# Optimization experiments

Measured on AMD Instinct MI355X. Metric: run time of the kernel, lower is better.

## Reference

```python
import jax, jax.numpy as jnp
import numpy as np

SQRT_D = 8.0

def setup_inputs() -> dict:
    key = jax.random.key(0)
    kq, kk, kv = jax.random.split(key, 3)
    shape = (2, 16, 2048, 64)  # [batch, heads, seq, head_dim]
    return {
        "q": jax.random.normal(kq, shape, dtype=jnp.float32),
        "k": jax.random.normal(kk, shape, dtype=jnp.float32),
        "v": jax.random.normal(kv, shape, dtype=jnp.float32),
    }

def reference(q, k, v):
    # score = softmax(QK^T / sqrt_d) over the key axis j
    scores = jnp.einsum('bhif,bhjf->bhij', q, k) / SQRT_D
    probs = jax.nn.softmax(scores, axis=-1)
    # Note: original returns output permuted to [b, i, h, f]
    attn = jnp.einsum('bhij,bhjf->bihf', probs, v)
    return attn
```

## Files before the change

kernel.cpp:

```cpp
#include <hip/hip_runtime.h>

#define S_LEN 2048
#define HEADS 16
#define DIM 64

typedef __attribute__((ext_vector_type(8))) short short8;
typedef __attribute__((ext_vector_type(16))) float float16v;
typedef __attribute__((ext_vector_type(4))) float float4v;
typedef __attribute__((ext_vector_type(4))) unsigned uint4v;

static __device__ __forceinline__ unsigned pkbf(float lo, float hi) {
  unsigned r;
  asm("v_cvt_pk_bf16_f32 %0, %1, %2" : "=v"(r) : "v"(lo), "v"(hi));
  return r;
}

static __device__ __forceinline__ void gll16(const short* g, short* l) {
  __builtin_amdgcn_global_load_lds(
      (const __attribute__((address_space(1))) void*)g,
      (__attribute__((address_space(3))) void*)l, 16, 0, 0);
}

static __device__ __forceinline__ void bar() {
  asm volatile("" ::: "memory");
  __builtin_amdgcn_s_barrier();
  asm volatile("" ::: "memory");
}

__global__ __launch_bounds__(256) void prep(const float* __restrict__ kk,
                                            const float* __restrict__ vv,
                                            short* __restrict__ kb,
                                            short* __restrict__ vt) {
  __shared__ unsigned t32[64 * 33];
  const int bx = blockIdx.x;
  const int bh = bx >> 5;
  const int j0 = (bx & 31) * 64;
  const int tid = threadIdx.x;

  {
    const int j = tid >> 2, f0 = (tid & 3) * 16;
    const float4v* src = (const float4v*)(kk + ((size_t)bh * S_LEN + j0 + j) * DIM + f0);
    float4v a0 = src[0], a1 = src[1], a2 = src[2], a3 = src[3];
    uint4v w0, w1;
    w0[0] = pkbf(a0[0], a0[1]); w0[1] = pkbf(a0[2], a0[3]);
    w0[2] = pkbf(a1[0], a1[1]); w0[3] = pkbf(a1[2], a1[3]);
    w1[0] = pkbf(a2[0], a2[1]); w1[1] = pkbf(a2[2], a2[3]);
    w1[2] = pkbf(a3[0], a3[1]); w1[3] = pkbf(a3[2], a3[3]);
    short* dstb = kb + (size_t)bh * (S_LEN * DIM) +
                  ((j0 >> 5) + (j >> 5)) * 2048 + (f0 >> 4) * 512 + (j & 31) * 8;
    *(uint4v*)dstb = w0;
    *(uint4v*)(dstb + 256) = w1;
  }
  {
    const int jp = (tid & 31) * 2, f0 = (tid >> 5) * 8;
    const int pp = ((jp & ~12) | ((jp & 4) << 1) | ((jp & 8) >> 1)) >> 1;
    const float* r0 = vv + ((size_t)bh * S_LEN + j0 + jp) * DIM + f0;
    const float* r1 = r0 + DIM;
    float4v a0 = *(const float4v*)r0, a1 = *(const float4v*)(r0 + 4);
    float4v b0 = *(const float4v*)r1, b1 = *(const float4v*)(r1 + 4);
#pragma unroll
    for (int e = 0; e < 4; e++) {
      t32[(f0 + e) * 33 + pp]     = pkbf(a0[e], b0[e]);
      t32[(f0 + 4 + e) * 33 + pp] = pkbf(a1[e], b1[e]);
    }
  }
  __syncthreads();
  {
    const int f = tid >> 2, x0 = (tid & 3) * 8;
    uint4v c0 = *(const uint4v*)&t32[f * 33 + x0];
    uint4v c1 = *(const uint4v*)&t32[f * 33 + x0 + 4];
    const int jt = (j0 >> 5) + (x0 >> 4);
    const int qd = (f >> 5) * 2 + ((x0 >> 3) & 1);
    short* dstb = vt + (size_t)bh * (S_LEN * DIM) + jt * 2048 + qd * 512 + (f & 31) * 8;
    *(uint4v*)dstb = c0;
    *(uint4v*)(dstb + 256) = c1;
  }
}

__global__ __launch_bounds__(256, 2) void attn_fwd(const float* __restrict__ q,
                                                   const short* __restrict__ kb,
                                                   const short* __restrict__ vt,
                                                   float* __restrict__ out) {
  __shared__ alignas(16) short lds[16384];
  const int bx0 = blockIdx.x;
  const int bx = (bx0 & 7) * 64 + (bx0 >> 3);
  const int bh = bx >> 4, it = bx & 15;
  const int b = bh >> 4, h = bh & 15;
  const int tid = threadIdx.x;
  const int w = tid >> 6, lane = tid & 63;
  const int n = lane & 31, hf = lane >> 5;
  const int i0 = it * 128 + w * 32;

  short8 qa[4];
  {
    const float sc = 0.125f * 1.44269504088896f;
    const float* qr = q + ((size_t)bh * S_LEN + i0 + n) * DIM + hf * 8;
#pragma unroll
    for (int ks = 0; ks < 4; ks++) {
      float4v x0 = *(const float4v*)(qr + ks * 16);
      float4v x1 = *(const float4v*)(qr + ks * 16 + 4);
      uint4v pk_;
      pk_[0] = pkbf(x0[0] * sc, x0[1] * sc); pk_[1] = pkbf(x0[2] * sc, x0[3] * sc);
      pk_[2] = pkbf(x1[0] * sc, x1[1] * sc); pk_[3] = pkbf(x1[2] * sc, x1[3] * sc);
      qa[ks] = *(short8*)&pk_;
    }
  }

  const short* kbase = kb + (size_t)bh * (S_LEN * DIM);
  const short* vbase = vt + (size_t)bh * (S_LEN * DIM);

  float16v zz;
#pragma unroll
  for (int e = 0; e < 16; e++) zz[e] = 0.f;
  float16v a0 = zz, a1 = zz;
  float lpa = 0.f, lpb = 0.f;

  auto stage = [&](short* dst, int t) {
    const int jt = 2 * t;
#pragma unroll
    for (int s = 0; s < 2; ++s) {
      gll16(kbase + (size_t)(jt + s) * 2048 + w * 512 + lane * 8, dst + s * 2048 + w * 512);
      gll16(vbase + (size_t)(jt + s) * 2048 + w * 512 + lane * 8, dst + 4096 + s * 2048 + w * 512);
    }
  };

  auto compute = [&](const short* kl, const short* vl) {
    short8 kf0 = *(const short8*)(kl + lane * 8);
    short8 kf1 = *(const short8*)(kl + 512 + lane * 8);
    short8 kf2 = *(const short8*)(kl + 1024 + lane * 8);
    short8 kf3 = *(const short8*)(kl + 1536 + lane * 8);
    __builtin_amdgcn_s_setprio(1);
    float16v sa = __builtin_amdgcn_mfma_f32_32x32x16_bf16(kf0, qa[0], zz, 0, 0, 0);
    float16v sb = __builtin_amdgcn_mfma_f32_32x32x16_bf16(kf2, qa[2], zz, 0, 0, 0);
    sa = __builtin_amdgcn_mfma_f32_32x32x16_bf16(kf1, qa[1], sa, 0, 0, 0);
    sb = __builtin_amdgcn_mfma_f32_32x32x16_bf16(kf3, qa[3], sb, 0, 0, 0);
    __builtin_amdgcn_s_setprio(0);
    float16v st;
#pragma unroll
    for (int e = 0; e < 16; e++) st[e] = __builtin_amdgcn_exp2f(sa[e] + sb[e]);
#pragma unroll
    for (int e = 0; e < 8; e++) { lpa += st[2 * e]; lpb += st[2 * e + 1]; }
    uint4v pb0, pb1;
#pragma unroll
    for (int u = 0; u < 4; u++) {
      pb0[u] = pkbf(st[2 * u], st[2 * u + 1]);
      pb1[u] = pkbf(st[8 + 2 * u], st[8 + 2 * u + 1]);
    }
    short8 p0 = *(short8*)&pb0, p1 = *(short8*)&pb1;
    short8 vf0 = *(const short8*)(vl + lane * 8);
    short8 vf1 = *(const short8*)(vl + 512 + lane * 8);
    short8 vf2 = *(const short8*)(vl + 1024 + lane * 8);
    short8 vf3 = *(const short8*)(vl + 1536 + lane * 8);
    __builtin_amdgcn_s_setprio(1);
    a0 = __builtin_amdgcn_mfma_f32_32x32x16_bf16(vf0, p0, a0, 0, 0, 0);
    a1 = __builtin_amdgcn_mfma_f32_32x32x16_bf16(vf2, p0, a1, 0, 0, 0);
    a0 = __builtin_amdgcn_mfma_f32_32x32x16_bf16(vf1, p1, a0, 0, 0, 0);
    a1 = __builtin_amdgcn_mfma_f32_32x32x16_bf16(vf3, p1, a1, 0, 0, 0);
    __builtin_amdgcn_s_setprio(0);
  };

  stage(lds, 0);
#pragma unroll 1
  for (int t = 0; t < 32; ++t) {
    short* cur = lds + (t & 1) * 8192;
    if (t < 31) {
      stage(lds + ((t + 1) & 1) * 8192, t + 1);
      asm volatile("s_waitcnt vmcnt(4)" ::: "memory");
    } else {
      asm volatile("s_waitcnt vmcnt(0)" ::: "memory");
    }
    bar();
    compute(cur, cur + 4096);
    compute(cur + 2048, cur + 4096 + 2048);
    bar();
  }

  float d = lpa + lpb;
  d += __shfl_xor(d, 32);
  const float inv = 1.f / d;

  float* const tb = (float*)lds + w * 1056;
  {
#pragma unroll
    for (int c = 0; c < 4; c++) {
      float4v u;
#pragma unroll
      for (int e = 0; e < 4; e++) u[e] = a0[4 * c + e] * inv;
      *(float4v*)&tb[n * 33 + 8 * c + 4 * hf] = u;
    }
    const int il = lane >> 1, fq = (lane & 1) * 16;
    const float* src = &tb[il * 33 + fq];
    float* dst = out + (((size_t)b * S_LEN + i0 + il) * HEADS + h) * DIM + fq;
#pragma unroll
    for (int u = 0; u < 4; u++) ((float4v*)dst)[u] = ((const float4v*)src)[u];
  }
  {
#pragma unroll
    for (int c = 0; c < 4; c++) {
      float4v u;
#pragma unroll
      for (int e = 0; e < 4; e++) u[e] = a1[4 * c + e] * inv;
      *(float4v*)&tb[n * 33 + 8 * c + 4 * hf] = u;
    }
    const int il = lane >> 1, fq = (lane & 1) * 16;
    const float* src = &tb[il * 33 + fq];
    float* dst = out + (((size_t)b * S_LEN + i0 + il) * HEADS + h) * DIM + 32 + fq;
#pragma unroll
    for (int u = 0; u < 4; u++) ((float4v*)dst)[u] = ((const float4v*)src)[u];
  }
}

extern "C" void kernel_launch(void* const* d_in, const int* in_sizes, int n_in,
                              void* d_out, int out_size, void* d_ws, size_t ws_size,
                              hipStream_t stream) {
  const float* q = (const float*)d_in[0];
  const float* k = (const float*)d_in[1];
  const float* v = (const float*)d_in[2];
  float* out = (float*)d_out;
  short* kb = (short*)d_ws;
  short* vt = (short*)d_ws + (size_t)32 * S_LEN * DIM;

  prep<<<1024, 256, 0, stream>>>(k, v, kb, vt);
  attn_fwd<<<512, 256, 0, stream>>>(q, kb, vt, out);
}
```

Before: 137.7 us.

## Load K/V fragments directly into registers, drop LDS staging and barriers

Replaces the LDS double-buffered global_load_lds staging with per-wave register prefetch of K and V fragments straight from global memory, with the loads for the next tile issued after the current MFMAs. Blocks shrink to 128 threads (two waves) and the grid doubles to 1024, removing the block-wide barriers. Each wave now reads the full K/V stream on its own, so global/L2 traffic roughly doubles compared with the shared LDS tiles, and more registers are held live for the prefetched fragments.

New measurement: 137.4 us. Within noise of the previous version (-0.2%).

```diff
diff --git a/kernel.cpp b/kernel.cpp
--- a/kernel.cpp
+++ b/kernel.cpp
@@ -13,18 +13,6 @@
   unsigned r;
   asm("v_cvt_pk_bf16_f32 %0, %1, %2" : "=v"(r) : "v"(lo), "v"(hi));
   return r;
-}
-
-static __device__ __forceinline__ void gll16(const short* g, short* l) {
-  __builtin_amdgcn_global_load_lds(
-      (const __attribute__((address_space(1))) void*)g,
-      (__attribute__((address_space(3))) void*)l, 16, 0, 0);
-}
-
-static __device__ __forceinline__ void bar() {
-  asm volatile("" ::: "memory");
-  __builtin_amdgcn_s_barrier();
-  asm volatile("" ::: "memory");
 }
 
 __global__ __launch_bounds__(256) void prep(const float* __restrict__ kk,
@@ -77,19 +65,19 @@
   }
 }
 
-__global__ __launch_bounds__(256, 2) void attn_fwd(const float* __restrict__ q,
+__global__ __launch_bounds__(128, 2) void attn_fwd(const float* __restrict__ q,
                                                    const short* __restrict__ kb,
                                                    const short* __restrict__ vt,
                                                    float* __restrict__ out) {
-  __shared__ alignas(16) short lds[16384];
+  __shared__ alignas(16) float smem[2 * 1056];
   const int bx0 = blockIdx.x;
-  const int bx = (bx0 & 7) * 64 + (bx0 >> 3);
-  const int bh = bx >> 4, it = bx & 15;
+  const int bx = (bx0 & 7) * 128 + (bx0 >> 3);
+  const int bh = bx >> 5, iblk = bx & 31;
   const int b = bh >> 4, h = bh & 15;
   const int tid = threadIdx.x;
   const int w = tid >> 6, lane = tid & 63;
   const int n = lane & 31, hf = lane >> 5;
-  const int i0 = it * 128 + w * 32;
+  const int i0 = iblk * 64 + w * 32;
 
   short8 qa[4];
   {
@@ -106,8 +94,17 @@
     }
   }
 
-  const short* kbase = kb + (size_t)bh * (S_LEN * DIM);
-  const short* vbase = vt + (size_t)bh * (S_LEN * DIM);
+  const short* kp = kb + (size_t)bh * (S_LEN * DIM) + lane * 8;
+  const short* vp = vt + (size_t)bh * (S_LEN * DIM) + lane * 8;
+
+  short8 kfA[4], kfB[4], vfA[4], vfB[4];
+#pragma unroll
+  for (int u = 0; u < 4; u++) {
+    kfA[u] = *(const short8*)(kp + u * 512);
+    kfB[u] = *(const short8*)(kp + 2048 + u * 512);
+    vfA[u] = *(const short8*)(vp + u * 512);
+    vfB[u] = *(const short8*)(vp + 2048 + u * 512);
+  }
 
   float16v zz;
 #pragma unroll
@@ -115,71 +112,76 @@
   float16v a0 = zz, a1 = zz;
   float lpa = 0.f, lpb = 0.f;
 
-  auto stage = [&](short* dst, int t) {
-    const int jt = 2 * t;
-#pragma unroll
-    for (int s = 0; s < 2; ++s) {
-      gll16(kbase + (size_t)(jt + s) * 2048 + w * 512 + lane * 8, dst + s * 2048 + w * 512);
-      gll16(vbase + (size_t)(jt + s) * 2048 + w * 512 + lane * 8, dst + 4096 + s * 2048 + w * 512);
-    }
-  };
-
-  auto compute = [&](const short* kl, const short* vl) {
-    short8 kf0 = *(const short8*)(kl + lane * 8);
-    short8 kf1 = *(const short8*)(kl + 512 + lane * 8);
-    short8 kf2 = *(const short8*)(kl + 1024 + lane * 8);
-    short8 kf3 = *(const short8*)(kl + 1536 + lane * 8);
-    __builtin_amdgcn_s_setprio(1);
-    float16v sa = __builtin_amdgcn_mfma_f32_32x32x16_bf16(kf0, qa[0], zz, 0, 0, 0);
-    float16v sb = __builtin_amdgcn_mfma_f32_32x32x16_bf16(kf2, qa[2], zz, 0, 0, 0);
-    sa = __builtin_amdgcn_mfma_f32_32x32x16_bf16(kf1, qa[1], sa, 0, 0, 0);
-    sb = __builtin_amdgcn_mfma_f32_32x32x16_bf16(kf3, qa[3], sb, 0, 0, 0);
-    __builtin_amdgcn_s_setprio(0);
-    float16v st;
-#pragma unroll
-    for (int e = 0; e < 16; e++) st[e] = __builtin_amdgcn_exp2f(sa[e] + sb[e]);
-#pragma unroll
-    for (int e = 0; e < 8; e++) { lpa += st[2 * e]; lpb += st[2 * e + 1]; }
-    uint4v pb0, pb1;
-#pragma unroll
-    for (int u = 0; u < 4; u++) {
-      pb0[u] = pkbf(st[2 * u], st[2 * u + 1]);
-      pb1[u] = pkbf(st[8 + 2 * u], st[8 + 2 * u + 1]);
-    }
-    short8 p0 = *(short8*)&pb0, p1 = *(short8*)&pb1;
-    short8 vf0 = *(const short8*)(vl + lane * 8);
-    short8 vf1 = *(const short8*)(vl + 512 + lane * 8);
-    short8 vf2 = *(const short8*)(vl + 1024 + lane * 8);
-    short8 vf3 = *(const short8*)(vl + 1536 + lane * 8);
-    __builtin_amdgcn_s_setprio(1);
-    a0 = __builtin_amdgcn_mfma_f32_32x32x16_bf16(vf0, p0, a0, 0, 0, 0);
-    a1 = __builtin_amdgcn_mfma_f32_32x32x16_bf16(vf2, p0, a1, 0, 0, 0);
-    a0 = __builtin_amdgcn_mfma_f32_32x32x16_bf16(vf1, p1, a0, 0, 0, 0);
-    a1 = __builtin_amdgcn_mfma_f32_32x32x16_bf16(vf3, p1, a1, 0, 0, 0);
-    __builtin_amdgcn_s_setprio(0);
-  };
-
-  stage(lds, 0);
 #pragma unroll 1
   for (int t = 0; t < 32; ++t) {
-    short* cur = lds + (t & 1) * 8192;
-    if (t < 31) {
-      stage(lds + ((t + 1) & 1) * 8192, t + 1);
-      asm volatile("s_waitcnt vmcnt(4)" ::: "memory");
-    } else {
-      asm volatile("s_waitcnt vmcnt(0)" ::: "memory");
-    }
-    bar();
-    compute(cur, cur + 4096);
-    compute(cur + 2048, cur + 4096 + 2048);
-    bar();
+    const int adv = (t < 31) ? 4096 : 0;
+    __builtin_amdgcn_s_setprio(1);
+    float16v sA = __builtin_amdgcn_mfma_f32_32x32x16_bf16(kfA[0], qa[0], zz, 0, 0, 0);
+    float16v sB = __builtin_amdgcn_mfma_f32_32x32x16_bf16(kfB[0], qa[0], zz, 0, 0, 0);
+    sA = __builtin_amdgcn_mfma_f32_32x32x16_bf16(kfA[1], qa[1], sA, 0, 0, 0);
+    sB = __builtin_amdgcn_mfma_f32_32x32x16_bf16(kfB[1], qa[1], sB, 0, 0, 0);
+    sA = __builtin_amdgcn_mfma_f32_32x32x16_bf16(kfA[2], qa[2], sA, 0, 0, 0);
+    sB = __builtin_amdgcn_mfma_f32_32x32x16_bf16(kfB[2], qa[2], sB, 0, 0, 0);
+    sA = __builtin_amdgcn_mfma_f32_32x32x16_bf16(kfA[3], qa[3], sA, 0, 0, 0);
+    sB = __builtin_amdgcn_mfma_f32_32x32x16_bf16(kfB[3], qa[3], sB, 0, 0, 0);
+    __builtin_amdgcn_s_setprio(0);
+    kp += adv;
+#pragma unroll
+    for (int u = 0; u < 4; u++) {
+      kfA[u] = *(const short8*)(kp + u * 512);
+      kfB[u] = *(const short8*)(kp + 2048 + u * 512);
+    }
+
+#pragma unroll
+    for (int e = 0; e < 16; e++) sA[e] = __builtin_amdgcn_exp2f(sA[e]);
+#pragma unroll
+    for (int e = 0; e < 8; e++) { lpa += sA[2 * e]; lpb += sA[2 * e + 1]; }
+    uint4v pA0, pA1;
+#pragma unroll
+    for (int u = 0; u < 4; u++) {
+      pA0[u] = pkbf(sA[2 * u], sA[2 * u + 1]);
+      pA1[u] = pkbf(sA[8 + 2 * u], sA[8 + 2 * u + 1]);
+    }
+    short8 a_p0 = *(short8*)&pA0, a_p1 = *(short8*)&pA1;
+
+    __builtin_amdgcn_s_setprio(1);
+    a0 = __builtin_amdgcn_mfma_f32_32x32x16_bf16(vfA[0], a_p0, a0, 0, 0, 0);
+    a1 = __builtin_amdgcn_mfma_f32_32x32x16_bf16(vfA[2], a_p0, a1, 0, 0, 0);
+    a0 = __builtin_amdgcn_mfma_f32_32x32x16_bf16(vfA[1], a_p1, a0, 0, 0, 0);
+    a1 = __builtin_amdgcn_mfma_f32_32x32x16_bf16(vfA[3], a_p1, a1, 0, 0, 0);
+    __builtin_amdgcn_s_setprio(0);
+
+#pragma unroll
+    for (int e = 0; e < 16; e++) sB[e] = __builtin_amdgcn_exp2f(sB[e]);
+#pragma unroll
+    for (int e = 0; e < 8; e++) { lpa += sB[2 * e]; lpb += sB[2 * e + 1]; }
+    uint4v pB0, pB1;
+#pragma unroll
+    for (int u = 0; u < 4; u++) {
+      pB0[u] = pkbf(sB[2 * u], sB[2 * u + 1]);
+      pB1[u] = pkbf(sB[8 + 2 * u], sB[8 + 2 * u + 1]);
+    }
+    short8 b_p0 = *(short8*)&pB0, b_p1 = *(short8*)&pB1;
+
+    __builtin_amdgcn_s_setprio(1);
+    a0 = __builtin_amdgcn_mfma_f32_32x32x16_bf16(vfB[0], b_p0, a0, 0, 0, 0);
+    a1 = __builtin_amdgcn_mfma_f32_32x32x16_bf16(vfB[2], b_p0, a1, 0, 0, 0);
+    a0 = __builtin_amdgcn_mfma_f32_32x32x16_bf16(vfB[1], b_p1, a0, 0, 0, 0);
+    a1 = __builtin_amdgcn_mfma_f32_32x32x16_bf16(vfB[3], b_p1, a1, 0, 0, 0);
+    __builtin_amdgcn_s_setprio(0);
+    vp += adv;
+#pragma unroll
+    for (int u = 0; u < 4; u++) {
+      vfA[u] = *(const short8*)(vp + u * 512);
+      vfB[u] = *(const short8*)(vp + 2048 + u * 512);
+    }
   }
 
   float d = lpa + lpb;
   d += __shfl_xor(d, 32);
   const float inv = 1.f / d;
 
-  float* const tb = (float*)lds + w * 1056;
+  float* const tb = smem + w * 1056;
   {
 #pragma unroll
     for (int c = 0; c < 4; c++) {
@@ -221,5 +223,5 @@
   short* vt = (short*)d_ws + (size_t)32 * S_LEN * DIM;
 
   prep<<<1024, 256, 0, stream>>>(k, v, kb, vt);
-  attn_fwd<<<512, 256, 0, stream>>>(q, kb, vt, out);
-}
+  attn_fwd<<<1024, 128, 0, stream>>>(q, kb, vt, out);
+}
```
